# Performance work log

Hardware: AMD Instinct MI355X
Metric: run time of the kernel (lower is better)

The kernel has to match this reference:

```python
import jax, jax.numpy as jnp
import numpy as np


def setup_inputs() -> dict:
    key = jax.random.key(0)
    k1, k2, k3 = jax.random.split(key, 3)
    n, c, h, w = 32, 384, 56, 56
    m, d_model = 8, 768
    x = jax.random.normal(k1, (n, c, h, w), dtype=jnp.float32)
    global_feature = jax.random.normal(k2, (n, m, d_model), dtype=jnp.float32)
    # Linear(d_model, 2*c): torch weight shape (2c, d_model)
    W_kv = jax.random.normal(k3, (2 * c, d_model), dtype=jnp.float32) * (1.0 / np.sqrt(d_model))
    b_kv = jnp.zeros((2 * c,), dtype=jnp.float32)
    return {"x": x, "global_feature": global_feature, "W_kv": W_kv, "b_kv": b_kv}


def reference(x, global_feature, W_kv, b_kv):
    n, c, h, w = x.shape
    # MLP (single Linear + ReLU6, no BN since bn=False)
    kv = jnp.einsum('nmd,ed->nme', global_feature, W_kv) + b_kv  # [n, m, 2c]
    kv = jnp.clip(kv, 0.0, 6.0)  # ReLU6
    K = kv[:, :, :c]   # [n, m, c]
    V = kv[:, :, c:]   # [n, m, c]
    q = x.reshape(n, c, h * w).transpose(0, 2, 1)  # [n, hw, c]
    scores = jnp.einsum('nqc,nkc->nqk', q, K)       # [n, hw, m] (unscaled)
    attn = jax.nn.softmax(scores, axis=-1)
    v_agg = jnp.einsum('nqk,nkc->nqc', attn, V)     # [n, hw, c]
    feature = v_agg.transpose(0, 2, 1).reshape(n, c, h, w)
    return feature + x
```

## Files before the change

### kernel.cpp

```cpp
#include <hip/hip_runtime.h>


#define NC 384
#define HWP 3136
#define DD 768
#define MM 8
#define EE 768

__global__ __launch_bounds__(256) void kv_kernel(const float* __restrict__ gf,
                                                 const float* __restrict__ Wk,
                                                 const float* __restrict__ bk,
                                                 float* __restrict__ kv) {
    __shared__ float g[MM * DD];
    const int n = blockIdx.y;
    const int et = blockIdx.x;
    const int t = threadIdx.x;

    const float* gfn = gf + (size_t)n * (MM * DD);
    for (int i = t; i < MM * DD; i += 256) g[i] = gfn[i];
    __syncthreads();

    const int e = et * 64 + (t & 63);
    const int mb = (t >> 6) * 2;

    const float4* w4 = (const float4*)(Wk + (size_t)e * DD);
    const float4* g0 = (const float4*)(g + (mb + 0) * DD);
    const float4* g1 = (const float4*)(g + (mb + 1) * DD);

    float a0 = 0.f, a1 = 0.f;
    #pragma unroll 8
    for (int i = 0; i < DD / 4; ++i) {
        const float4 w = w4[i];
        const float4 v0 = g0[i];
        const float4 v1 = g1[i];
        a0 += w.x * v0.x + w.y * v0.y + w.z * v0.z + w.w * v0.w;
        a1 += w.x * v1.x + w.y * v1.y + w.z * v1.z + w.w * v1.w;
    }
    const float bv = bk[e];
    float* o = kv + (size_t)n * (MM * EE);
    o[(mb + 0) * EE + e] = fminf(fmaxf(a0 + bv, 0.f), 6.f);
    o[(mb + 1) * EE + e] = fminf(fmaxf(a1 + bv, 0.f), 6.f);
}

__global__ __launch_bounds__(256, 4) void attn_kernel(const float* __restrict__ x,
                                                      const float* __restrict__ kv,
                                                      float* __restrict__ out) {
    __shared__ float kvs[7168];
    __shared__ float sc[4][8][32];

    const int n = blockIdx.y;
    const int tile = blockIdx.x;
    const int t = threadIdx.x;
    const int p2 = t & 15;
    const int gq = t >> 4;
    const int w = t >> 6;
    const int c0 = gq * 24;
    const int pos0 = tile * 32 + p2 * 2;

    const float4* kvn4 = (const float4*)(kv + (size_t)n * (MM * EE));
    #pragma unroll
    for (int r = 0; r < 6; ++r) {
        const int f = t + r * 256;
        const int k = f / 192;
        const int e4 = f - k * 192;
        const int half = (e4 >= 96) ? 1 : 0;
        const int c4 = e4 - half * 96;
        const int g = c4 / 6;
        const int j4 = c4 - g * 6;
        *(float4*)&kvs[half * 3584 + k * 448 + g * 28 + j4 * 4] = kvn4[f];
    }

    const float* xp = x + (size_t)n * NC * HWP + (size_t)c0 * HWP + pos0;
    float2 xr[24];
    #pragma unroll
    for (int i = 0; i < 24; ++i) xr[i] = *(const float2*)(xp + (size_t)i * HWP);

    __syncthreads();

    float accx[8], accy[8];
    #pragma unroll
    for (int k = 0; k < 8; ++k) { accx[k] = 0.f; accy[k] = 0.f; }

    #pragma unroll
    for (int i4 = 0; i4 < 6; ++i4) {
        const float2 x0 = xr[i4 * 4 + 0];
        const float2 x1 = xr[i4 * 4 + 1];
        const float2 x2 = xr[i4 * 4 + 2];
        const float2 x3 = xr[i4 * 4 + 3];
        #pragma unroll
        for (int k = 0; k < 8; ++k) {
            const float4 kk = *(const float4*)&kvs[k * 448 + gq * 28 + i4 * 4];
            accx[k] += x0.x * kk.x + x1.x * kk.y + x2.x * kk.z + x3.x * kk.w;
            accy[k] += x0.y * kk.x + x1.y * kk.y + x2.y * kk.z + x3.y * kk.w;
        }
    }

    #pragma unroll
    for (int k = 0; k < 8; ++k) {
        accx[k] += __shfl_xor(accx[k], 16, 64);
        accx[k] += __shfl_xor(accx[k], 32, 64);
        accy[k] += __shfl_xor(accy[k], 16, 64);
        accy[k] += __shfl_xor(accy[k], 32, 64);
    }
    if ((t & 48) == 0) {
        #pragma unroll
        for (int k = 0; k < 8; ++k)
            *(float2*)&sc[w][k][p2 * 2] = make_float2(accx[k], accy[k]);
    }
    __syncthreads();

    float sx[8], sy[8];
    #pragma unroll
    for (int k = 0; k < 8; ++k) {
        float2 s = *(const float2*)&sc[0][k][p2 * 2];
        #pragma unroll
        for (int ww = 1; ww < 4; ++ww) {
            const float2 q = *(const float2*)&sc[ww][k][p2 * 2];
            s.x += q.x; s.y += q.y;
        }
        sx[k] = s.x; sy[k] = s.y;
    }
    {
        float mx = sx[0], my = sy[0];
        #pragma unroll
        for (int k = 1; k < 8; ++k) { mx = fmaxf(mx, sx[k]); my = fmaxf(my, sy[k]); }
        float sux = 0.f, suy = 0.f;
        #pragma unroll
        for (int k = 0; k < 8; ++k) {
            sx[k] = __expf(sx[k] - mx); sux += sx[k];
            sy[k] = __expf(sy[k] - my); suy += sy[k];
        }
        const float ix = 1.f / sux, iy = 1.f / suy;
        #pragma unroll
        for (int k = 0; k < 8; ++k) { sx[k] *= ix; sy[k] *= iy; }
    }

    float* op = out + (size_t)n * NC * HWP + (size_t)c0 * HWP + pos0;
    #pragma unroll
    for (int i4 = 0; i4 < 6; ++i4) {
        float2 o0 = xr[i4 * 4 + 0];
        float2 o1 = xr[i4 * 4 + 1];
        float2 o2 = xr[i4 * 4 + 2];
        float2 o3 = xr[i4 * 4 + 3];
        #pragma unroll
        for (int k = 0; k < 8; ++k) {
            const float4 vv = *(const float4*)&kvs[3584 + k * 448 + gq * 28 + i4 * 4];
            o0.x += sx[k] * vv.x; o0.y += sy[k] * vv.x;
            o1.x += sx[k] * vv.y; o1.y += sy[k] * vv.y;
            o2.x += sx[k] * vv.z; o2.y += sy[k] * vv.z;
            o3.x += sx[k] * vv.w; o3.y += sy[k] * vv.w;
        }
        *(float2*)(op + (size_t)(i4 * 4 + 0) * HWP) = o0;
        *(float2*)(op + (size_t)(i4 * 4 + 1) * HWP) = o1;
        *(float2*)(op + (size_t)(i4 * 4 + 2) * HWP) = o2;
        *(float2*)(op + (size_t)(i4 * 4 + 3) * HWP) = o3;
    }
}

extern "C" void kernel_launch(void* const* d_in, const int* in_sizes, int n_in,
                              void* d_out, int out_size, void* d_ws, size_t ws_size,
                              hipStream_t stream) {
    const float* x  = (const float*)d_in[0];
    const float* gf = (const float*)d_in[1];
    const float* Wk = (const float*)d_in[2];
    const float* bk = (const float*)d_in[3];
    float* out = (float*)d_out;
    float* kv = (float*)d_ws;

    kv_kernel<<<dim3(12, 32), 256, 0, stream>>>(gf, Wk, bk, kv);
    attn_kernel<<<dim3(98, 32), 256, 0, stream>>>(x, kv, out);
}
```

Before: 320.1 us.

## Remap attention threads so each wavefront owns whole positions, drop shared-memory score reduction

Reassigns work in the attention kernel: each wavefront now covers 8 positions with 8 channel groups of 48 channels, so the full score reduction happens with wavefront shuffles instead of a cross-wave shared-memory pass and an extra barrier. The shared K/V layout is repacked to match the 48-channel groups, and the launch bound is raised to 6 blocks per SIMD-equivalent to push occupancy. In exchange, x loads and output stores become scalar 4-byte accesses (8 consecutive positions per group) instead of float2, which may reduce memory coalescing efficiency on this bandwidth-bound kernel. The x loads also move after the barrier, giving up their overlap with the K/V staging.

```diff
diff --git a/kernel.cpp b/kernel.cpp
--- a/kernel.cpp
+++ b/kernel.cpp
@@ -42,20 +42,19 @@
     o[(mb + 1) * EE + e] = fminf(fmaxf(a1 + bv, 0.f), 6.f);
 }
 
-__global__ __launch_bounds__(256, 4) void attn_kernel(const float* __restrict__ x,
+__global__ __launch_bounds__(256, 6) void attn_kernel(const float* __restrict__ x,
                                                       const float* __restrict__ kv,
                                                       float* __restrict__ out) {
-    __shared__ float kvs[7168];
-    __shared__ float sc[4][8][32];
+    __shared__ float kvs[6656];
 
     const int n = blockIdx.y;
     const int tile = blockIdx.x;
     const int t = threadIdx.x;
-    const int p2 = t & 15;
-    const int gq = t >> 4;
+    const int lane = t & 63;
     const int w = t >> 6;
-    const int c0 = gq * 24;
-    const int pos0 = tile * 32 + p2 * 2;
+    const int g = lane >> 3;
+    const int pos = tile * 32 + w * 8 + (lane & 7);
+    const int c0 = g * 48;
 
     const float4* kvn4 = (const float4*)(kv + (size_t)n * (MM * EE));
     #pragma unroll
@@ -65,95 +64,74 @@
         const int e4 = f - k * 192;
         const int half = (e4 >= 96) ? 1 : 0;
         const int c4 = e4 - half * 96;
-        const int g = c4 / 6;
-        const int j4 = c4 - g * 6;
-        *(float4*)&kvs[half * 3584 + k * 448 + g * 28 + j4 * 4] = kvn4[f];
+        const int g2 = c4 / 12;
+        const int j4 = c4 - g2 * 12;
+        *(float4*)&kvs[half * 3328 + k * 416 + g2 * 52 + j4 * 4] = kvn4[f];
     }
-
-    const float* xp = x + (size_t)n * NC * HWP + (size_t)c0 * HWP + pos0;
-    float2 xr[24];
-    #pragma unroll
-    for (int i = 0; i < 24; ++i) xr[i] = *(const float2*)(xp + (size_t)i * HWP);
-
     __syncthreads();
 
-    float accx[8], accy[8];
+    const float* xp = x + (size_t)n * NC * HWP + (size_t)c0 * HWP + pos;
+    float xr[48];
     #pragma unroll
-    for (int k = 0; k < 8; ++k) { accx[k] = 0.f; accy[k] = 0.f; }
+    for (int i = 0; i < 48; ++i) xr[i] = xp[(size_t)i * HWP];
 
+    float acc[8];
     #pragma unroll
-    for (int i4 = 0; i4 < 6; ++i4) {
-        const float2 x0 = xr[i4 * 4 + 0];
-        const float2 x1 = xr[i4 * 4 + 1];
-        const float2 x2 = xr[i4 * 4 + 2];
-        const float2 x3 = xr[i4 * 4 + 3];
+    for (int k = 0; k < 8; ++k) acc[k] = 0.f;
+
+    const float* kbase = &kvs[g * 52];
+    #pragma unroll
+    for (int i4 = 0; i4 < 12; ++i4) {
+        const float x0 = xr[i4 * 4 + 0];
+        const float x1 = xr[i4 * 4 + 1];
+        const float x2 = xr[i4 * 4 + 2];
+        const float x3 = xr[i4 * 4 + 3];
         #pragma unroll
         for (int k = 0; k < 8; ++k) {
-            const float4 kk = *(const float4*)&kvs[k * 448 + gq * 28 + i4 * 4];
-            accx[k] += x0.x * kk.x + x1.x * kk.y + x2.x * kk.z + x3.x * kk.w;
-            accy[k] += x0.y * kk.x + x1.y * kk.y + x2.y * kk.z + x3.y * kk.w;
+            const float4 kk = *(const float4*)&kbase[k * 416 + i4 * 4];
+            acc[k] += x0 * kk.x + x1 * kk.y + x2 * kk.z + x3 * kk.w;
         }
     }
 
     #pragma unroll
     for (int k = 0; k < 8; ++k) {
-        accx[k] += __shfl_xor(accx[k], 16, 64);
-        accx[k] += __shfl_xor(accx[k], 32, 64);
-        accy[k] += __shfl_xor(accy[k], 16, 64);
-        accy[k] += __shfl_xor(accy[k], 32, 64);
+        acc[k] += __shfl_xor(acc[k], 8, 64);
+        acc[k] += __shfl_xor(acc[k], 16, 64);
+        acc[k] += __shfl_xor(acc[k], 32, 64);
     }
-    if ((t & 48) == 0) {
+
+    {
+        float mx = acc[0];
         #pragma unroll
-        for (int k = 0; k < 8; ++k)
-            *(float2*)&sc[w][k][p2 * 2] = make_float2(accx[k], accy[k]);
+        for (int k = 1; k < 8; ++k) mx = fmaxf(mx, acc[k]);
+        float su = 0.f;
+        #pragma unroll
+        for (int k = 0; k < 8; ++k) { acc[k] = __expf(acc[k] - mx); su += acc[k]; }
+        const float inv = 1.f / su;
+        #pragma unroll
+        for (int k = 0; k < 8; ++k) acc[k] *= inv;
     }
-    __syncthreads();
 
-    float sx[8], sy[8];
+    float* op = out + (size_t)n * NC * HWP + (size_t)c0 * HWP + pos;
+    const float* vbase = &kvs[3328 + g * 52];
     #pragma unroll
-    for (int k = 0; k < 8; ++k) {
-        float2 s = *(const float2*)&sc[0][k][p2 * 2];
-        #pragma unroll
-        for (int ww = 1; ww < 4; ++ww) {
-            const float2 q = *(const float2*)&sc[ww][k][p2 * 2];
-            s.x += q.x; s.y += q.y;
-        }
-        sx[k] = s.x; sy[k] = s.y;
-    }
-    {
-        float mx = sx[0], my = sy[0];
-        #pragma unroll
-        for (int k = 1; k < 8; ++k) { mx = fmaxf(mx, sx[k]); my = fmaxf(my, sy[k]); }
-        float sux = 0.f, suy = 0.f;
+    for (int i4 = 0; i4 < 12; ++i4) {
+        float o0 = xr[i4 * 4 + 0];
+        float o1 = xr[i4 * 4 + 1];
+        float o2 = xr[i4 * 4 + 2];
+        float o3 = xr[i4 * 4 + 3];
         #pragma unroll
         for (int k = 0; k < 8; ++k) {
-            sx[k] = __expf(sx[k] - mx); sux += sx[k];
-            sy[k] = __expf(sy[k] - my); suy += sy[k];
+            const float4 vv = *(const float4*)&vbase[k * 416 + i4 * 4];
+            o0 += acc[k] * vv.x;
+            o1 += acc[k] * vv.y;
+            o2 += acc[k] * vv.z;
+            o3 += acc[k] * vv.w;
         }
-        const float ix = 1.f / sux, iy = 1.f / suy;
-        #pragma unroll
-        for (int k = 0; k < 8; ++k) { sx[k] *= ix; sy[k] *= iy; }
-    }
-
-    float* op = out + (size_t)n * NC * HWP + (size_t)c0 * HWP + pos0;
-    #pragma unroll
-    for (int i4 = 0; i4 < 6; ++i4) {
-        float2 o0 = xr[i4 * 4 + 0];
-        float2 o1 = xr[i4 * 4 + 1];
-        float2 o2 = xr[i4 * 4 + 2];
-        float2 o3 = xr[i4 * 4 + 3];
-        #pragma unroll
-        for (int k = 0; k < 8; ++k) {
-            const float4 vv = *(const float4*)&kvs[3584 + k * 448 + gq * 28 + i4 * 4];
-            o0.x += sx[k] * vv.x; o0.y += sy[k] * vv.x;
-            o1.x += sx[k] * vv.y; o1.y += sy[k] * vv.y;
-            o2.x += sx[k] * vv.z; o2.y += sy[k] * vv.z;
-            o3.x += sx[k] * vv.w; o3.y += sy[k] * vv.w;
-        }
-        *(float2*)(op + (size_t)(i4 * 4 + 0) * HWP) = o0;
-        *(float2*)(op + (size_t)(i4 * 4 + 1) * HWP) = o1;
-        *(float2*)(op + (size_t)(i4 * 4 + 2) * HWP) = o2;
-        *(float2*)(op + (size_t)(i4 * 4 + 3) * HWP) = o3;
+        op[(size_t)(i4 * 4 + 0) * HWP] = o0;
+        op[(size_t)(i4 * 4 + 1) * HWP] = o1;
+        op[(size_t)(i4 * 4 + 2) * HWP] = o2;
+        op[(size_t)(i4 * 4 + 3) * HWP] = o3;
     }
 }
 
```

Result: slower. 359.2 us (+12.2%).
